# Performance work log

Hardware: AMD Instinct MI355X
Metric: run time of the kernel (lower is better)

## Reference

```python
import jax, jax.numpy as jnp
import numpy as np

EPS = 1e-5

def layer_norm(x, gamma, beta):
    mu = jnp.mean(x, axis=-1, keepdims=True)
    var = jnp.var(x, axis=-1, keepdims=True)
    return (x - mu) * jax.lax.rsqrt(var + EPS) * gamma + beta

def setup_inputs() -> dict:
    key = jax.random.key(0)
    ks = jax.random.split(key, 9)
    B, S, H = 4, 4096, 1024
    x = jax.random.normal(ks[0], (B, S, H), dtype=jnp.float32)
    w1 = jax.random.normal(ks[1], (H, 4 * H), dtype=jnp.float32) * (1.0 / np.sqrt(H))
    b1 = jnp.zeros((4 * H,), dtype=jnp.float32)
    w2 = jax.random.normal(ks[2], (4 * H, H), dtype=jnp.float32) * (1.0 / np.sqrt(4 * H))
    b2 = jnp.zeros((H,), dtype=jnp.float32)
    g1 = jnp.ones((H,), dtype=jnp.float32)
    be1 = jnp.zeros((H,), dtype=jnp.float32)
    g2 = jnp.ones((H,), dtype=jnp.float32)
    be2 = jnp.zeros((H,), dtype=jnp.float32)
    return {"x": x, "w1": w1, "b1": b1, "w2": w2, "b2": b2,
            "g1": g1, "be1": be1, "g2": g2, "be2": be2}

def reference(x, w1, b1, w2, b2, g1, be1, g2, be2):
    # FNet mixing: FFT over hidden dim, then seq dim, take real part
    x_ft = jnp.fft.fft(jnp.fft.fft(x.astype(jnp.float32), axis=-1), axis=-2).real
    h = layer_norm(x + x_ft, g1, be1)
    # FFN with exact GELU (torch nn.GELU default); dropout is identity in eval
    ffn = jax.nn.gelu(h @ w1 + b1, approximate=False) @ w2 + b2
    return layer_norm(h + ffn, g2, be2)
```

## Files before the change

### kernel.cpp

```cpp
#include <hip/hip_runtime.h>
#include <math.h>
#include <stdint.h>

#define DI __device__ __forceinline__
typedef unsigned short u16;
typedef unsigned int   u32;
typedef unsigned long long u64;

typedef __attribute__((ext_vector_type(4))) float f32x4;
typedef __attribute__((ext_vector_type(8))) short bf16x8;

DI float bf2f(u16 v){ return __uint_as_float(((u32)v) << 16); }
DI u16 f2bf(float f){ u32 u = __float_as_uint(f); return (u16)((u + 0x7FFFu + ((u >> 16) & 1u)) >> 16); }
DI u32 pack2(float re, float im){ return (u32)f2bf(re) | ((u32)f2bf(im) << 16); }

DI float gelu_fast(float v){
  float t = v * v;
  float z = v * fmaf(0.0356774081f, t, 0.7978845608f);
  z = fminf(z, 15.0f);
  float e = __expf(2.0f * z);
  return v * e * __frcp_rn(1.0f + e);
}

__global__ __launch_bounds__(256) void transpose_u32(const u32* __restrict__ in, u32* __restrict__ out, int R, int C){
  __shared__ u32 tile[64][65];
  int t = threadIdx.x;
  int c = t & 63, r0 = t >> 6;
  size_t bofs = (size_t)blockIdx.z * (size_t)R * (size_t)C;
  const u32* ib = in  + bofs + (size_t)(blockIdx.y * 64) * C + blockIdx.x * 64;
  u32*       ob = out + bofs + (size_t)(blockIdx.x * 64) * R + blockIdx.y * 64;
  #pragma unroll
  for (int i = 0; i < 16; i++){ int r = r0 + i * 4; tile[r][c] = ib[(size_t)r * C + c]; }
  __syncthreads();
  #pragma unroll
  for (int i = 0; i < 16; i++){ int r = r0 + i * 4; ob[(size_t)r * R + c] = tile[c][r]; }
}

__global__ __launch_bounds__(256) void transpose_f32_bf16(const float* __restrict__ in, u16* __restrict__ out, int R, int C){
  __shared__ u16 tile[64][65];
  int t = threadIdx.x;
  int c = t & 63, r0 = t >> 6;
  const float* ib = in  + (size_t)(blockIdx.y * 64) * C + blockIdx.x * 64;
  u16*         ob = out + (size_t)(blockIdx.x * 64) * R + blockIdx.y * 64;
  #pragma unroll
  for (int i = 0; i < 16; i++){ int r = r0 + i * 4; tile[r][c] = f2bf(ib[(size_t)r * C + c]); }
  __syncthreads();
  #pragma unroll
  for (int i = 0; i < 16; i++){ int r = r0 + i * 4; ob[(size_t)r * R + c] = tile[c][r]; }
}

template<int LOGN>
DI float2* fft_r4(float2* s, float2* d, int t){
  const int Q = 1 << (LOGN - 2);
  #pragma unroll
  for (int st = 0; st < (LOGN >> 1); ++st){
    const int m = 1 << (2 * st);
    const float ang = -6.28318530717958647692f * (float)m / (float)(1 << LOGN);
    #pragma unroll
    for (int j0 = 0; j0 < Q; j0 += 256){
      int j = j0 + t;
      int p = j >> (2 * st);
      int q = j & (m - 1);
      int o = q + (p << (2 * st + 2));
      float2 a0 = s[j], a1 = s[j + Q], a2 = s[j + 2 * Q], a3 = s[j + 3 * Q];
      float s0r = a0.x + a2.x, s0i = a0.y + a2.y, d0r = a0.x - a2.x, d0i = a0.y - a2.y;
      float s1r = a1.x + a3.x, s1i = a1.y + a3.y, d1r = a1.x - a3.x, d1i = a1.y - a3.y;
      float sn, cs; __sincosf(ang * (float)p, &sn, &cs);
      float t2r = cs * cs - sn * sn, t2i = 2.f * cs * sn;
      float t3r = t2r * cs - t2i * sn, t3i = t2r * sn + t2i * cs;
      float e1r = d0r + d1i, e1i = d0i - d1r;
      float e2r = s0r - s1r, e2i = s0i - s1i;
      float e3r = d0r - d1i, e3i = d0i + d1r;
      d[o]         = make_float2(s0r + s1r, s0i + s1i);
      d[o + m]     = make_float2(cs * e1r - sn * e1i,  cs * e1i + sn * e1r);
      d[o + 2 * m] = make_float2(t2r * e2r - t2i * e2i, t2r * e2i + t2i * e2r);
      d[o + 3 * m] = make_float2(t3r * e3r - t3i * e3i, t3r * e3i + t3i * e3r);
    }
    __syncthreads();
    float2* tp = s; s = d; d = tp;
  }
  return s;
}

__global__ __launch_bounds__(256) void fft_seq(const float* __restrict__ xT, u32* __restrict__ ZT2,
                                               float* __restrict__ Zny){
  __shared__ float2 A[4096], Bb[4096];
  int t = threadIdx.x, g = blockIdx.x;
  const float* r0 = xT + (size_t)(2 * g) * 4096;
  #pragma unroll
  for (int i = 0; i < 4; i++){
    int idx = i * 1024 + t * 4;
    float4 va = *(const float4*)(r0 + idx);
    float4 vb = *(const float4*)(r0 + 4096 + idx);
    A[idx + 0] = make_float2(va.x, vb.x);
    A[idx + 1] = make_float2(va.y, vb.y);
    A[idx + 2] = make_float2(va.z, vb.z);
    A[idx + 3] = make_float2(va.w, vb.w);
  }
  __syncthreads();
  float2* R = fft_r4<12>(A, Bb, t);
  size_t ob0 = (size_t)(2 * g) * 2048;
  #pragma unroll
  for (int i = 0; i < 2; i++){
    int k0 = i * 1024 + t * 4;
    u32 wa[4], wb[4];
    #pragma unroll
    for (int kk = 0; kk < 4; kk++){
      int k = k0 + kk, m = (4096 - k) & 4095;
      float2 zk = R[k], zm = R[m];
      wa[kk] = pack2(0.5f * (zk.x + zm.x), 0.5f * (zk.y - zm.y));
      wb[kk] = pack2(0.5f * (zk.y + zm.y), 0.5f * (zm.x - zk.x));
    }
    *(uint4*)(ZT2 + ob0 + k0)        = make_uint4(wa[0], wa[1], wa[2], wa[3]);
    *(uint4*)(ZT2 + ob0 + 2048 + k0) = make_uint4(wb[0], wb[1], wb[2], wb[3]);
  }
  if (t == 0){ float2 z = R[2048]; Zny[2 * g] = z.x; Zny[2 * g + 1] = z.y; }
}

DI void block_stats4(float a1, float a2, float b1, float b2, int t,
                     float& mA, float& iA, float& mB, float& iB){
  __shared__ float sh[4][4];
  #pragma unroll
  for (int o = 32; o > 0; o >>= 1){
    a1 += __shfl_down(a1, o); a2 += __shfl_down(a2, o);
    b1 += __shfl_down(b1, o); b2 += __shfl_down(b2, o);
  }
  if ((t & 63) == 0){ int w = t >> 6; sh[w][0] = a1; sh[w][1] = a2; sh[w][2] = b1; sh[w][3] = b2; }
  __syncthreads();
  float SA = sh[0][0] + sh[1][0] + sh[2][0] + sh[3][0];
  float QA = sh[0][1] + sh[1][1] + sh[2][1] + sh[3][1];
  float SB = sh[0][2] + sh[1][2] + sh[2][2] + sh[3][2];
  float QB = sh[0][3] + sh[1][3] + sh[2][3] + sh[3][3];
  mA = SA * (1.f / 1024.f); iA = rsqrtf(QA * (1.f / 1024.f) - mA * mA + 1e-5f);
  mB = SB * (1.f / 1024.f); iB = rsqrtf(QB * (1.f / 1024.f) - mB * mB + 1e-5f);
}

__global__ __launch_bounds__(256) void fft_hid_ln(const u32* __restrict__ Z2, const float* __restrict__ Zny,
    const float* __restrict__ x, const float* __restrict__ g1, const float* __restrict__ be1,
    u16* __restrict__ h){
  __shared__ float2 A[1024], Bb[1024];
  int t = threadIdx.x, id = blockIdx.x;
  int b = id / 2049, k = id - b * 2049;
  int idx = t * 4;
  if (k == 2048){
    float4 v = *(const float4*)(Zny + b * 1024 + idx);
    A[idx + 0] = make_float2(v.x, 0.f); A[idx + 1] = make_float2(v.y, 0.f);
    A[idx + 2] = make_float2(v.z, 0.f); A[idx + 3] = make_float2(v.w, 0.f);
  } else {
    uint4 zv = *(const uint4*)(Z2 + ((size_t)b * 2048 + k) * 1024 + idx);
    A[idx + 0] = make_float2(bf2f((u16)(zv.x & 0xffffu)), bf2f((u16)(zv.x >> 16)));
    A[idx + 1] = make_float2(bf2f((u16)(zv.y & 0xffffu)), bf2f((u16)(zv.y >> 16)));
    A[idx + 2] = make_float2(bf2f((u16)(zv.z & 0xffffu)), bf2f((u16)(zv.z >> 16)));
    A[idx + 3] = make_float2(bf2f((u16)(zv.w & 0xffffu)), bf2f((u16)(zv.w >> 16)));
  }
  __syncthreads();
  float2* R = fft_r4<10>(A, Bb, t);
  int rowA = b * 4096 + k;
  bool two = (k >= 1) && (k <= 2047);
  int rowB = b * 4096 + (4096 - k);
  float4 xa = *(const float4*)(x + (size_t)rowA * 1024 + idx);
  float vA0 = R[idx + 0].x + xa.x, vA1 = R[idx + 1].x + xa.y;
  float vA2 = R[idx + 2].x + xa.z, vA3 = R[idx + 3].x + xa.w;
  float vB0 = 0.f, vB1 = 0.f, vB2 = 0.f, vB3 = 0.f;
  if (two){
    float4 xb = *(const float4*)(x + (size_t)rowB * 1024 + idx);
    vB0 = R[(1024 - (idx + 0)) & 1023].x + xb.x;
    vB1 = R[(1024 - (idx + 1)) & 1023].x + xb.y;
    vB2 = R[(1024 - (idx + 2)) & 1023].x + xb.z;
    vB3 = R[(1024 - (idx + 3)) & 1023].x + xb.w;
  }
  float mA, iA, mB, iB;
  block_stats4(vA0 + vA1 + vA2 + vA3, vA0 * vA0 + vA1 * vA1 + vA2 * vA2 + vA3 * vA3,
               vB0 + vB1 + vB2 + vB3, vB0 * vB0 + vB1 * vB1 + vB2 * vB2 + vB3 * vB3,
               t, mA, iA, mB, iB);
  float4 gv = *(const float4*)(g1 + idx);
  float4 bv = *(const float4*)(be1 + idx);
  ushort4 oA;
  oA.x = f2bf((vA0 - mA) * iA * gv.x + bv.x);
  oA.y = f2bf((vA1 - mA) * iA * gv.y + bv.y);
  oA.z = f2bf((vA2 - mA) * iA * gv.z + bv.z);
  oA.w = f2bf((vA3 - mA) * iA * gv.w + bv.w);
  *(ushort4*)(h + (size_t)rowA * 1024 + idx) = oA;
  if (two){
    ushort4 oB;
    oB.x = f2bf((vB0 - mB) * iB * gv.x + bv.x);
    oB.y = f2bf((vB1 - mB) * iB * gv.y + bv.y);
    oB.z = f2bf((vB2 - mB) * iB * gv.z + bv.z);
    oB.w = f2bf((vB3 - mB) * iB * gv.w + bv.w);
    *(ushort4*)(h + (size_t)rowB * 1024 + idx) = oB;
  }
}

__global__ __launch_bounds__(256) void ln_rows(const u16* __restrict__ yv, const float* __restrict__ g,
    const float* __restrict__ be, float* __restrict__ o){
  int t = threadIdx.x;
  size_t base = (size_t)blockIdx.x * 1024;
  int idx = t * 4;
  ushort4 v4 = *(const ushort4*)(yv + base + idx);
  float v0 = bf2f(v4.x), v1 = bf2f(v4.y), v2 = bf2f(v4.z), v3 = bf2f(v4.w);
  float mA, iA, mB, iB;
  block_stats4(v0 + v1 + v2 + v3, v0 * v0 + v1 * v1 + v2 * v2 + v3 * v3, 0.f, 0.f, t, mA, iA, mB, iB);
  float4 gv = *(const float4*)(g + idx);
  float4 bv = *(const float4*)(be + idx);
  float4 ov;
  ov.x = (v0 - mA) * iA * gv.x + bv.x;
  ov.y = (v1 - mA) * iA * gv.y + bv.y;
  ov.z = (v2 - mA) * iA * gv.z + bv.z;
  ov.w = (v3 - mA) * iA * gv.w + bv.w;
  *(float4*)(o + base + idx) = ov;
}

typedef const __attribute__((address_space(1))) void* as1cp;
typedef __attribute__((address_space(3))) void* as3p;
DI void async_copy16(const void* g, void* l){
  __builtin_amdgcn_global_load_lds((as1cp)(u64)g, (as3p)(u32)(u64)l, 16, 0, 0);
}
DI void bar(){
  asm volatile("" ::: "memory");
  __builtin_amdgcn_s_barrier();
  asm volatile("" ::: "memory");
}

template<int DOGELU>
__global__ __launch_bounds__(512, 2) void gemm256(const u16* __restrict__ A, const u16* __restrict__ Bm,
    const float* __restrict__ bias, const u16* __restrict__ resid, u16* __restrict__ C,
    int M, int N, int K, int gn_shift, int npg_shift, int mpg, int bpg, int npt)
{
  __shared__ u16 sA[2][2][8192];
  __shared__ u16 sB[2][2][8192];
  int t = threadIdx.x, wv = t >> 6, ln = t & 63;

  int bid = blockIdx.x;
  int c8 = bid & 7, j0 = bid >> 3;
  int ng = c8 & ((1 << gn_shift) - 1);
  int mg = c8 >> gn_shift;
  int npg_m1 = (1 << npg_shift) - 1;

  int wm = wv >> 2, wn = wv & 3;
  int lt = ln & 15;
  int cs = (((ln >> 4) ^ ((ln >> 1) & 3)) << 3);
  int arow = (wm * 128 + lt) * 32 + cs;
  int brow = (wn * 64 + lt) * 32 + cs;
  int srow = wv * 32 + (ln >> 2);
  int gch  = ((ln & 3) ^ ((srow >> 1) & 3)) << 3;
  int ldof = wv * 1024 + ln * 8;
  int NT = K >> 6;

  #define STAGE(g0, g1, kc, unit) do{ \
    async_copy16((g0) + (kc), (unit) + ldof); \
    async_copy16((g1) + (kc), (unit) + 512 + ldof); }while(0)
  #define PROLOGUE() do{ \
    STAGE(gA0, gA1, 0,  &sA[0][0][0]); \
    STAGE(gB0, gB1, 0,  &sB[0][0][0]); \
    STAGE(gA0, gA1, 32, &sA[0][1][0]); \
    STAGE(gB0, gB1, 32, &sB[0][1][0]); \
    STAGE(gA0, gA1, 64, &sA[1][0][0]); \
    STAGE(gB0, gB1, 64, &sB[1][0][0]); \
    STAGE(gA0, gA1, 96, &sA[1][1][0]); }while(0)

  int jt = j0;
  int n0 = (((ng << npg_shift) + (jt & npg_m1)) << 8);
  int m0 = ((mg * mpg + (jt >> npg_shift)) << 8);
  const u16* gA0 = A  + (size_t)(m0 + srow) * K + gch;
  const u16* gA1 = gA0 + (size_t)16 * K;
  const u16* gB0 = Bm + (size_t)(n0 + srow) * K + gch;
  const u16* gB1 = gB0 + (size_t)16 * K;
  PROLOGUE();
  asm volatile("s_waitcnt vmcnt(6)" ::: "memory");
  bar();

  for (int s = 0; s < npt; ++s){
    f32x4 acc[8][4];
    #pragma unroll
    for (int mf = 0; mf < 8; mf++)
      #pragma unroll
      for (int nf = 0; nf < 4; nf++) acc[mf][nf] = (f32x4){0.f, 0.f, 0.f, 0.f};

    for (int kt = 0; kt < NT; ++kt){
      int buf = kt & 1;
      u16* a0s = &sA[buf][0][0];
      u16* a1s = &sA[buf][1][0];
      u16* b0s = &sB[buf][0][0];
      u16* b1s = &sB[buf][1][0];
      u16* bn1 = &sB[buf ^ 1][1][0];
      bool st1 = (kt + 1) < NT;
      bool st2 = (kt + 2) < NT;
      int kb1 = (kt + 1) << 6, kb2 = (kt + 2) << 6;
      bf16x8 af1[8], af2[8], b1r[4], b2r[4];

      #pragma unroll
      for (int mf = 0; mf < 8; mf++) af1[mf] = *(const bf16x8*)(a0s + arow + mf * 512);
      #pragma unroll
      for (int nf = 0; nf < 4; nf++) b1r[nf] = *(const bf16x8*)(b0s + brow + nf * 512);
      if (st1) STAGE(gB0, gB1, kb1 + 32, bn1);
      bar();
      __builtin_amdgcn_s_setprio(1);
      #pragma unroll
      for (int mf = 0; mf < 8; mf++){
        acc[mf][0] = __builtin_amdgcn_mfma_f32_16x16x32_bf16(af1[mf], b1r[0], acc[mf][0], 0, 0, 0);
        acc[mf][1] = __builtin_amdgcn_mfma_f32_16x16x32_bf16(af1[mf], b1r[1], acc[mf][1], 0, 0, 0);
      }
      __builtin_amdgcn_s_setprio(0);
      bar();

      #pragma unroll
      for (int mf = 0; mf < 8; mf++) af2[mf] = *(const bf16x8*)(a1s + arow + mf * 512);
      #pragma unroll
      for (int nf = 0; nf < 4; nf++) b2r[nf] = *(const bf16x8*)(b1s + brow + nf * 512);
      if (st2) STAGE(gA0, gA1, kb2, a0s);
      bar();
      __builtin_amdgcn_s_setprio(1);
      #pragma unroll
      for (int mf = 0; mf < 8; mf++){
        acc[mf][2] = __builtin_amdgcn_mfma_f32_16x16x32_bf16(af1[mf], b1r[2], acc[mf][2], 0, 0, 0);
        acc[mf][3] = __builtin_amdgcn_mfma_f32_16x16x32_bf16(af1[mf], b1r[3], acc[mf][3], 0, 0, 0);
      }
      __builtin_amdgcn_s_setprio(0);
      asm volatile("s_waitcnt lgkmcnt(0)" ::: "memory");
      bar();

      if (st2) STAGE(gB0, gB1, kb2, b0s);
      bar();
      __builtin_amdgcn_s_setprio(1);
      #pragma unroll
      for (int mf = 0; mf < 8; mf++){
        acc[mf][0] = __builtin_amdgcn_mfma_f32_16x16x32_bf16(af2[mf], b2r[0], acc[mf][0], 0, 0, 0);
        acc[mf][1] = __builtin_amdgcn_mfma_f32_16x16x32_bf16(af2[mf], b2r[1], acc[mf][1], 0, 0, 0);
      }
      __builtin_amdgcn_s_setprio(0);
      bar();

      if (st2) STAGE(gA0, gA1, kb2 + 32, a1s);
      bar();
      __builtin_amdgcn_s_setprio(1);
      #pragma unroll
      for (int mf = 0; mf < 8; mf++){
        acc[mf][2] = __builtin_amdgcn_mfma_f32_16x16x32_bf16(af2[mf], b2r[2], acc[mf][2], 0, 0, 0);
        acc[mf][3] = __builtin_amdgcn_mfma_f32_16x16x32_bf16(af2[mf], b2r[3], acc[mf][3], 0, 0, 0);
      }
      __builtin_amdgcn_s_setprio(0);
      if (st2) asm volatile("s_waitcnt vmcnt(6)" ::: "memory");
      else     asm volatile("s_waitcnt vmcnt(0)" ::: "memory");
      bar();
    }

    int em0 = m0, en0 = n0;
    if (s + 1 < npt){
      jt = j0 + (s + 1) * bpg;
      n0 = (((ng << npg_shift) + (jt & npg_m1)) << 8);
      m0 = ((mg * mpg + (jt >> npg_shift)) << 8);
      gA0 = A  + (size_t)(m0 + srow) * K + gch;
      gA1 = gA0 + (size_t)16 * K;
      gB0 = Bm + (size_t)(n0 + srow) * K + gch;
      gB1 = gB0 + (size_t)16 * K;
      PROLOGUE();
    }

    int colq = lt, rq = ln >> 4;
    #pragma unroll
    for (int mf = 0; mf < 8; mf++){
      int mr = em0 + wm * 128 + mf * 16 + rq * 4;
      #pragma unroll
      for (int nf = 0; nf < 4; nf++){
        int col = en0 + wn * 64 + nf * 16 + colq;
        float bv = bias[col];
        #pragma unroll
        for (int i = 0; i < 4; i++){
          float v = acc[mf][nf][i] + bv;
          if (DOGELU){
            v = gelu_fast(v);
          } else {
            v += bf2f(resid[(size_t)(mr + i) * N + col]);
          }
          C[(size_t)(mr + i) * N + col] = f2bf(v);
        }
      }
    }

    if (s + 1 < npt){
      asm volatile("s_waitcnt vmcnt(6)" ::: "memory");
      bar();
    }
  }
  #undef PROLOGUE
  #undef STAGE
}

static inline int ilog2(int v){ int s = 0; while ((1 << s) < v) ++s; return s; }

extern "C" void kernel_launch(void* const* d_in, const int* in_sizes, int n_in,
                              void* d_out, int out_size, void* d_ws, size_t ws_size,
                              hipStream_t stream){
  const float* x   = (const float*)d_in[0];
  const float* w1  = (const float*)d_in[1];
  const float* b1  = (const float*)d_in[2];
  const float* w2  = (const float*)d_in[3];
  const float* b2  = (const float*)d_in[4];
  const float* g1  = (const float*)d_in[5];
  const float* be1 = (const float*)d_in[6];
  const float* g2  = (const float*)d_in[7];
  const float* be2 = (const float*)d_in[8];
  float* out = (float*)d_out;
  char* ws = (char*)d_ws;
  const size_t MB = (size_t)1 << 20;
  float* xT  = (float*)(ws);
  u32*  ZT2  = (u32*)(ws + 64 * MB);
  float* Zny = (float*)(ws + 96 * MB);
  u32*  Z2   = (u32*)(ws);
  u16*  h    = (u16*)(ws + 32 * MB);
  u16*  w1T  = (u16*)(ws + 64 * MB);
  u16*  w2T  = (u16*)(ws + 72 * MB);
  u16*  u    = (u16*)(ws + 80 * MB);
  u16*  y    = (u16*)(ws);
  dim3 blk(256, 1, 1);
  dim3 blk2(512, 1, 1);

  transpose_u32<<<dim3(16, 64, 4), blk, 0, stream>>>((const u32*)x, (u32*)xT, 4096, 1024);
  fft_seq      <<<dim3(2048, 1, 1), blk, 0, stream>>>(xT, ZT2, Zny);
  transpose_u32<<<dim3(32, 16, 4), blk, 0, stream>>>(ZT2, Z2, 1024, 2048);
  fft_hid_ln   <<<dim3(4 * 2049, 1, 1), blk, 0, stream>>>(Z2, Zny, x, g1, be1, h);

  transpose_f32_bf16<<<dim3(64, 16, 1), blk, 0, stream>>>(w1, w1T, 1024, 4096);
  transpose_f32_bf16<<<dim3(16, 64, 1), blk, 0, stream>>>(w2, w2T, 4096, 1024);
  int nch = (ws_size >= (size_t)209 * MB) ? 1 : (ws_size >= (size_t)145 * MB) ? 2 : 4;
  int Mc = 16384 / nch;
  for (int ch = 0; ch < nch; ++ch){
    const u16* hch = h + (size_t)ch * Mc * 1024;
    u16* ych = y + (size_t)ch * Mc * 1024;
    {
      int tm = Mc >> 8, tn = 16, gn = 2;
      int tiles = tm * tn;
      int grid = tiles < 256 ? tiles : 256;
      int npt = tiles / grid, bpg = grid >> 3;
      int npgs = ilog2(tn >> gn);
      int mpg = tm >> (3 - gn);
      gemm256<1><<<dim3(grid), blk2, 0, stream>>>(hch, w1T, b1, (const u16*)nullptr, u,
                                                  Mc, 4096, 1024, gn, npgs, mpg, bpg, npt);
    }
    {
      int tm = Mc >> 8, tn = 4, gn = 0;
      int tiles = tm * tn;
      int grid = tiles < 256 ? tiles : 256;
      int npt = tiles / grid, bpg = grid >> 3;
      int npgs = ilog2(tn >> gn);
      int mpg = tm >> (3 - gn);
      gemm256<0><<<dim3(grid), blk2, 0, stream>>>(u, w2T, b2, hch, ych,
                                                  Mc, 1024, 4096, gn, npgs, mpg, bpg, npt);
    }
  }
  ln_rows<<<dim3(16384, 1, 1), blk, 0, stream>>>(y, g2, be2, out);
}
```

Measured before the change: 546.6 us.

## Switch GEMM inner loop from 16x16x32 to 32x32x16 bf16 MFMA tiles

Replaces the 16x16x32 MFMA fragments with 32x32x16 MFMA instructions in the main GEMM kernel. The LDS fragment addressing, accumulator layout (f32x16 per 32x32 block) and epilogue row/column mapping change to match. The goal is fewer LDS reads per flop and higher MFMA throughput from the larger instruction shape. It also reorders when the second-half fragments are read and drops an explicit lgkmcnt wait, which shifts register pressure and the timing of LDS reads.

New measurement: 572.6 us. 1.05x slower.

```diff
diff --git a/kernel.cpp b/kernel.cpp
--- a/kernel.cpp
+++ b/kernel.cpp
@@ -7,8 +7,9 @@
 typedef unsigned int   u32;
 typedef unsigned long long u64;
 
-typedef __attribute__((ext_vector_type(4))) float f32x4;
-typedef __attribute__((ext_vector_type(8))) short bf16x8;
+typedef __attribute__((ext_vector_type(4)))  float f32x4;
+typedef __attribute__((ext_vector_type(16))) float f32x16;
+typedef __attribute__((ext_vector_type(8)))  short bf16x8;
 
 DI float bf2f(u16 v){ return __uint_as_float(((u32)v) << 16); }
 DI u16 f2bf(float f){ u32 u = __float_as_uint(f); return (u16)((u + 0x7FFFu + ((u >> 16) & 1u)) >> 16); }
@@ -237,10 +238,12 @@
   int npg_m1 = (1 << npg_shift) - 1;
 
   int wm = wv >> 2, wn = wv & 3;
-  int lt = ln & 15;
-  int cs = (((ln >> 4) ^ ((ln >> 1) & 3)) << 3);
-  int arow = (wm * 128 + lt) * 32 + cs;
-  int brow = (wn * 64 + lt) * 32 + cs;
+  int l32 = ln & 31, hi = ln >> 5;
+  int swzl = (ln >> 1) & 3;
+  int cb0 = ((0 | hi) ^ swzl) << 3;
+  int cb1 = ((2 | hi) ^ swzl) << 3;
+  int abase = (wm * 128 + l32) * 32;
+  int bbase = (wn * 64  + l32) * 32;
   int srow = wv * 32 + (ln >> 2);
   int gch  = ((ln & 3) ^ ((srow >> 1) & 3)) << 3;
   int ldof = wv * 1024 + ln * 8;
@@ -257,6 +260,23 @@
     STAGE(gA0, gA1, 64, &sA[1][0][0]); \
     STAGE(gB0, gB1, 64, &sB[1][0][0]); \
     STAGE(gA0, gA1, 96, &sA[1][1][0]); }while(0)
+  #define RD12(src_a, src_b) do{ \
+    _Pragma("unroll") \
+    for (int mfb = 0; mfb < 4; mfb++){ \
+      af[mfb]     = *(const bf16x8*)((src_a) + abase + mfb * 1024 + cb0); \
+      af[4 + mfb] = *(const bf16x8*)((src_a) + abase + mfb * 1024 + cb1); \
+    } \
+    bf[0] = *(const bf16x8*)((src_b) + bbase + cb0); \
+    bf[1] = *(const bf16x8*)((src_b) + bbase + cb1); \
+    bf[2] = *(const bf16x8*)((src_b) + bbase + 1024 + cb0); \
+    bf[3] = *(const bf16x8*)((src_b) + bbase + 1024 + cb1); }while(0)
+  #define MM8(nfb) do{ \
+    _Pragma("unroll") \
+    for (int mfb = 0; mfb < 4; mfb++) \
+      acc[mfb][nfb] = __builtin_amdgcn_mfma_f32_32x32x16_bf16(af[mfb], bf[2*(nfb)], acc[mfb][nfb], 0, 0, 0); \
+    _Pragma("unroll") \
+    for (int mfb = 0; mfb < 4; mfb++) \
+      acc[mfb][nfb] = __builtin_amdgcn_mfma_f32_32x32x16_bf16(af[4 + mfb], bf[2*(nfb) + 1], acc[mfb][nfb], 0, 0, 0); }while(0)
 
   int jt = j0;
   int n0 = (((ng << npg_shift) + (jt & npg_m1)) << 8);
@@ -270,11 +290,12 @@
   bar();
 
   for (int s = 0; s < npt; ++s){
-    f32x4 acc[8][4];
+    f32x16 acc[4][2];
     #pragma unroll
-    for (int mf = 0; mf < 8; mf++)
+    for (int mfb = 0; mfb < 4; mfb++)
       #pragma unroll
-      for (int nf = 0; nf < 4; nf++) acc[mf][nf] = (f32x4){0.f, 0.f, 0.f, 0.f};
+      for (int nfb = 0; nfb < 2; nfb++)
+        acc[mfb][nfb] = (f32x16)(0.f);
 
     for (int kt = 0; kt < NT; ++kt){
       int buf = kt & 1;
@@ -286,58 +307,35 @@
       bool st1 = (kt + 1) < NT;
       bool st2 = (kt + 2) < NT;
       int kb1 = (kt + 1) << 6, kb2 = (kt + 2) << 6;
-      bf16x8 af1[8], af2[8], b1r[4], b2r[4];
-
-      #pragma unroll
-      for (int mf = 0; mf < 8; mf++) af1[mf] = *(const bf16x8*)(a0s + arow + mf * 512);
-      #pragma unroll
-      for (int nf = 0; nf < 4; nf++) b1r[nf] = *(const bf16x8*)(b0s + brow + nf * 512);
+      bf16x8 af[8], bf[4];
+
+      RD12(a0s, b0s);
       if (st1) STAGE(gB0, gB1, kb1 + 32, bn1);
       bar();
       __builtin_amdgcn_s_setprio(1);
-      #pragma unroll
-      for (int mf = 0; mf < 8; mf++){
-        acc[mf][0] = __builtin_amdgcn_mfma_f32_16x16x32_bf16(af1[mf], b1r[0], acc[mf][0], 0, 0, 0);
-        acc[mf][1] = __builtin_amdgcn_mfma_f32_16x16x32_bf16(af1[mf], b1r[1], acc[mf][1], 0, 0, 0);
-      }
+      MM8(0);
       __builtin_amdgcn_s_setprio(0);
       bar();
 
-      #pragma unroll
-      for (int mf = 0; mf < 8; mf++) af2[mf] = *(const bf16x8*)(a1s + arow + mf * 512);
-      #pragma unroll
-      for (int nf = 0; nf < 4; nf++) b2r[nf] = *(const bf16x8*)(b1s + brow + nf * 512);
       if (st2) STAGE(gA0, gA1, kb2, a0s);
       bar();
       __builtin_amdgcn_s_setprio(1);
-      #pragma unroll
-      for (int mf = 0; mf < 8; mf++){
-        acc[mf][2] = __builtin_amdgcn_mfma_f32_16x16x32_bf16(af1[mf], b1r[2], acc[mf][2], 0, 0, 0);
-        acc[mf][3] = __builtin_amdgcn_mfma_f32_16x16x32_bf16(af1[mf], b1r[3], acc[mf][3], 0, 0, 0);
-      }
+      MM8(1);
       __builtin_amdgcn_s_setprio(0);
-      asm volatile("s_waitcnt lgkmcnt(0)" ::: "memory");
-      bar();
-
+      bar();
+
+      RD12(a1s, b1s);
       if (st2) STAGE(gB0, gB1, kb2, b0s);
       bar();
       __builtin_amdgcn_s_setprio(1);
-      #pragma unroll
-      for (int mf = 0; mf < 8; mf++){
-        acc[mf][0] = __builtin_amdgcn_mfma_f32_16x16x32_bf16(af2[mf], b2r[0], acc[mf][0], 0, 0, 0);
-        acc[mf][1] = __builtin_amdgcn_mfma_f32_16x16x32_bf16(af2[mf], b2r[1], acc[mf][1], 0, 0, 0);
-      }
+      MM8(0);
       __builtin_amdgcn_s_setprio(0);
       bar();
 
       if (st2) STAGE(gA0, gA1, kb2 + 32, a1s);
       bar();
       __builtin_amdgcn_s_setprio(1);
-      #pragma unroll
-      for (int mf = 0; mf < 8; mf++){
-        acc[mf][2] = __builtin_amdgcn_mfma_f32_16x16x32_bf16(af2[mf], b2r[2], acc[mf][2], 0, 0, 0);
-        acc[mf][3] = __builtin_amdgcn_mfma_f32_16x16x32_bf16(af2[mf], b2r[3], acc[mf][3], 0, 0, 0);
-      }
+      MM8(1);
       __builtin_amdgcn_s_setprio(0);
       if (st2) asm volatile("s_waitcnt vmcnt(6)" ::: "memory");
       else     asm volatile("s_waitcnt vmcnt(0)" ::: "memory");
@@ -356,23 +354,26 @@
       PROLOGUE();
     }
 
-    int colq = lt, rq = ln >> 4;
     #pragma unroll
-    for (int mf = 0; mf < 8; mf++){
-      int mr = em0 + wm * 128 + mf * 16 + rq * 4;
+    for (int mfb = 0; mfb < 4; mfb++){
       #pragma unroll
-      for (int nf = 0; nf < 4; nf++){
-        int col = en0 + wn * 64 + nf * 16 + colq;
+      for (int nfb = 0; nfb < 2; nfb++){
+        int col = en0 + wn * 64 + nfb * 32 + l32;
         float bv = bias[col];
         #pragma unroll
-        for (int i = 0; i < 4; i++){
-          float v = acc[mf][nf][i] + bv;
-          if (DOGELU){
-            v = gelu_fast(v);
-          } else {
-            v += bf2f(resid[(size_t)(mr + i) * N + col]);
+        for (int g4 = 0; g4 < 4; g4++){
+          #pragma unroll
+          for (int i = 0; i < 4; i++){
+            int row_l = i + 8 * g4 + 4 * hi;
+            int mr = em0 + wm * 128 + mfb * 32 + row_l;
+            float v = acc[mfb][nfb][g4 * 4 + i] + bv;
+            if (DOGELU){
+              v = gelu_fast(v);
+            } else {
+              v += bf2f(resid[(size_t)mr * N + col]);
+            }
+            C[(size_t)mr * N + col] = f2bf(v);
           }
-          C[(size_t)(mr + i) * N + col] = f2bf(v);
         }
       }
     }
@@ -382,6 +383,8 @@
       bar();
     }
   }
+  #undef MM8
+  #undef RD12
   #undef PROLOGUE
   #undef STAGE
 }
```
